# Kernel optimization log

Measured on AMD Instinct MI355X. Metric: run time of the kernel, lower is better.

The kernel has to match this reference:

```python
import jax, jax.numpy as jnp
import numpy as np

TOPK_CONF = 100   # cfg.nms_top_k_conf
TOPK_IOU = 15     # cfg.nms_top_k_iou
IOU_GAUSS = (32, 32)  # cfg.iou_gauss_dim
EPS = 1e-6        # cfg.positive


def unnormal_gaussian(mask_shape, loc):
    """loc: [..., 4] = (cx, cy, w, h) in [0,1). Returns [..., H, W] unnormalized gaussians."""
    H, W = mask_shape
    ys = (jnp.arange(H, dtype=loc.dtype) + 0.5) / H  # [H]
    xs = (jnp.arange(W, dtype=loc.dtype) + 0.5) / W  # [W]
    cx, cy = loc[..., 0], loc[..., 1]
    sx = jnp.abs(loc[..., 2]) * 0.5 + 1e-3
    sy = jnp.abs(loc[..., 3]) * 0.5 + 1e-3
    dx2 = (xs - cx[..., None]) ** 2 / (2.0 * sx[..., None] ** 2)  # [..., W]
    dy2 = (ys - cy[..., None]) ** 2 / (2.0 * sy[..., None] ** 2)  # [..., H]
    return jnp.exp(-(dy2[..., :, None] + dx2[..., None, :]))      # [..., H, W]


def setup_inputs() -> dict:
    key = jax.random.key(0)
    k1, k2, k3, k4, k5 = jax.random.split(key, 5)
    B, P, C, M = 4, 19248, 81, 32
    original = jax.random.normal(k1, (B, 3, 550, 550), dtype=jnp.float32)
    loc = jax.random.uniform(k2, (B, P, 4), dtype=jnp.float32)  # cx,cy,w,h in [0,1)
    conf = jax.random.normal(k3, (B, P, C), dtype=jnp.float32)
    mask = jax.random.normal(k4, (B, P, M), dtype=jnp.float32)
    proto = jax.random.normal(k5, (B, 138, 138, M), dtype=jnp.float32)
    return {"original": original, "loc": loc, "conf": conf, "mask": mask, "proto": proto}


def reference(original, loc, conf, mask, proto):
    B, H, W = original.shape[0], original.shape[2], original.shape[3]
    # class-1 foreground confidence after softmax over classes
    conf1 = jax.nn.softmax(conf, axis=2)[:, :, 1]  # [B, P]

    # ---- detect(): top-k by conf, pairwise gaussian IoU, keep lowest-overlap boxes ----
    order = jnp.argsort(-conf1, axis=-1)[:, :TOPK_CONF]                    # [B, K]
    sconf = jnp.take_along_axis(conf1, order, axis=1)                      # [B, K]
    sloc = jnp.take_along_axis(loc, order[..., None], axis=1)              # [B, K, 4]
    smask = jnp.take_along_axis(mask, order[..., None], axis=1)            # [B, K, Mdim]

    gauss = unnormal_gaussian(IOU_GAUSS, sloc)                             # [B, K, G, G]
    g_rows = gauss[:, None, :, :, :]                                       # broadcast [B,1,K,G,G]
    g_cols = gauss[:, :, None, :, :]                                       # broadcast [B,K,1,G,G]
    inter = jnp.sum(jnp.minimum(g_rows, g_cols), axis=(-2, -1))            # [B, K, K]
    union = jnp.sum(jnp.maximum(g_rows, g_cols), axis=(-2, -1))            # [B, K, K]
    gauss_iou = inter / union
    iou_max = jnp.max(jnp.triu(gauss_iou, k=1), axis=1)                    # [B, K]
    keep = jnp.argsort(iou_max, axis=-1)[:, :TOPK_IOU]                     # [B, Kk]

    kloc = jnp.take_along_axis(sloc, keep[..., None], axis=1)              # [B, Kk, 4]
    kmask = jnp.take_along_axis(smask, keep[..., None], axis=1)            # [B, Kk, Mdim]
    kconf = jnp.take_along_axis(sconf, keep, axis=1)                       # [B, Kk]

    # ---- VarianceLoss ----
    Hp, Wp = proto.shape[1], proto.shape[2]
    ug = unnormal_gaussian((Hp, Wp), kloc)                                 # [B, Kk, Hp, Wp]
    assembled = jax.nn.sigmoid(jnp.einsum('bhwm,bkm->bkhw', proto, kmask)) # lincomb + sigmoid
    attention = assembled * ug
    mask_conf = attention * kconf[:, :, None, None]                        # einsum('abcd,ab->abcd')
    denom = jnp.sum(mask_conf, axis=1, keepdims=True) + EPS
    final_conf = 1.0 - jnp.sum(mask_conf ** 2 / denom, axis=1)             # [B, Hp, Wp]
    final_conf = jnp.where(jnp.isnan(final_conf), 0.0, final_conf)

    resized = jax.image.resize(final_conf, (B, H, W), method='bilinear')   # [B, H, W]
    total_conf = jnp.sum(resized, axis=0)                                  # [H, W]
    weighted_mean = jnp.einsum('bchw,bhw->chw', original, resized)         # [C, H, W]
    squared_diff = (original - weighted_mean) ** 2
    weighted_diff = squared_diff * resized[:, None, :, :]                  # einsum('abcd,acd->abcd')
    weighted_var = weighted_diff / (total_conf + EPS)
    return jnp.sum(weighted_var) / 100.0
```

## Files before the change

### kernel.cpp

```cpp
#include <hip/hip_runtime.h>
#include <math.h>

#define B 4
#define P 19248
#define C 81
#define M 32
#define K1 100
#define K2 15
#define G 32
#define HP 138
#define HO 550
#define FEPS 1e-6f

#define NBUCKET 8192
#define CAP 2048

#define RROW 128
#define RSP 83

#define TI 16
#define NT 7
#define NTP 28
#define CH 128
#define NCH 8
#define SP 132

__global__ __launch_bounds__(128) void k_conf1(const float* __restrict__ conf,
                                               float* __restrict__ conf1) {
    int row0 = blockIdx.x * RROW;
    int nrows = min(RROW, B * P - row0);
    int tid = threadIdx.x;
    __shared__ float s_rows[RROW * RSP];
    const float* src = conf + (size_t)row0 * C;
    int total = nrows * C;
    for (int i = tid; i < total; i += 128) {
        int r = i / C, c2 = i - r * C;
        s_rows[r * RSP + c2] = src[i];
    }
    __syncthreads();
    if (tid < nrows) {
        const float* rw = &s_rows[tid * RSP];
        float m = rw[0];
#pragma unroll
        for (int i = 1; i < C; ++i) m = fmaxf(m, rw[i]);
        float s = 0.f, e1 = 0.f;
#pragma unroll
        for (int i = 0; i < C; ++i) {
            float e = expf(rw[i] - m);
            s += e;
            if (i == 1) e1 = e;
        }
        conf1[row0 + tid] = e1 / s;
    }
}

__global__ __launch_bounds__(1024) void k_hist(const float* __restrict__ conf1,
                                               unsigned int* __restrict__ ghist) {
    int b = blockIdx.y;
    int tid = threadIdx.x;
    __shared__ unsigned int lh[NBUCKET];
    for (int i = tid; i < NBUCKET; i += 1024) lh[i] = 0;
    __syncthreads();
    int p0 = blockIdx.x * (P / 8);
    for (int p = p0 + tid; p < p0 + P / 8; p += 1024) {
        unsigned int bits = __float_as_uint(conf1[(size_t)b * P + p]);
        atomicAdd(&lh[bits >> 17], 1u);
    }
    __syncthreads();
    for (int i = tid; i < NBUCKET; i += 1024) {
        unsigned int v = lh[i];
        if (v) atomicAdd(&ghist[b * NBUCKET + i], v);
    }
}

__global__ __launch_bounds__(1024) void k_select(
    const unsigned int* __restrict__ ghist, const float* __restrict__ conf1,
    const float* __restrict__ loc, const float* __restrict__ mask,
    float* __restrict__ sconf, float* __restrict__ sloc, float* __restrict__ smask) {
    int b = blockIdx.x;
    int tid = threadIdx.x;
    __shared__ unsigned int hist[NBUCKET];
    __shared__ unsigned int gsum_[1024];
    __shared__ unsigned int g2[64];
    __shared__ unsigned long long s_keys[CAP];
    __shared__ int s_T;
    __shared__ int s_cnt;
    __shared__ int   s_order[K1];
    __shared__ float s_conf[K1];

    for (int i = tid; i < NBUCKET; i += 1024) hist[i] = ghist[b * NBUCKET + i];
    if (tid == 0) s_cnt = 0;
    __syncthreads();
    {
        unsigned int gs = 0;
#pragma unroll
        for (int i = 0; i < 8; ++i) gs += hist[tid * 8 + i];
        gsum_[tid] = gs;
    }
    __syncthreads();
    if (tid < 64) {
        unsigned int gs = 0;
#pragma unroll
        for (int i = 0; i < 16; ++i) gs += gsum_[tid * 16 + i];
        g2[tid] = gs;
    }
    __syncthreads();
    if (tid < 64) {
        unsigned int v1 = g2[tid];
        unsigned int s1 = v1;
#pragma unroll
        for (int o = 1; o < 64; o <<= 1) {
            unsigned int x = __shfl_down(s1, o, 64);
            if (tid + o < 64) s1 += x;
        }
        unsigned long long m1 = __ballot((int)s1 >= K1);
        int S = 63 - __builtin_clzll(m1);
        int cum1 = (int)__shfl(s1, S, 64) - (int)__shfl(v1, S, 64);

        unsigned int v2 = (tid < 16) ? gsum_[S * 16 + tid] : 0u;
        unsigned int s2 = v2;
#pragma unroll
        for (int o = 1; o < 16; o <<= 1) {
            unsigned int x = __shfl_down(s2, o, 64);
            if (tid + o < 16) s2 += x;
        }
        unsigned long long m2 = __ballot((tid < 16) && (cum1 + (int)s2 >= K1));
        int r2 = 63 - __builtin_clzll(m2);
        int gI = S * 16 + r2;
        int cum2 = cum1 + (int)__shfl(s2, r2, 64) - (int)__shfl(v2, r2, 64);

        unsigned int v3 = (tid < 8) ? hist[gI * 8 + tid] : 0u;
        unsigned int s3 = v3;
#pragma unroll
        for (int o = 1; o < 8; o <<= 1) {
            unsigned int x = __shfl_down(s3, o, 64);
            if (tid + o < 8) s3 += x;
        }
        unsigned long long m3 = __ballot((tid < 8) && (cum2 + (int)s3 >= K1));
        int r3 = 63 - __builtin_clzll(m3);
        if (tid == 0) s_T = gI * 8 + r3;
    }
    __syncthreads();

    int T = s_T;
    for (int p = tid; p < P; p += 1024) {
        unsigned int bits = __float_as_uint(conf1[(size_t)b * P + p]);
        if ((int)(bits >> 17) >= T) {
            int pos = atomicAdd(&s_cnt, 1);
            if (pos < CAP)
                s_keys[pos] = ((unsigned long long)bits << 32)
                            | (unsigned int)(0xFFFFFFFFu - (unsigned int)p);
        }
    }
    __syncthreads();
    int nc = min(s_cnt, CAP);
    int ncp = (nc + 7) & ~7;
    if (tid < ncp - nc) s_keys[nc + tid] = 0ULL;
    __syncthreads();

    for (int t = tid; t < nc; t += 1024) {
        unsigned long long mk = s_keys[t];
        int rank = 0;
#pragma unroll 8
        for (int i = 0; i < ncp; ++i) rank += (s_keys[i] > mk);
        if (rank < K1) {
            s_order[rank] = (int)(0xFFFFFFFFu - (unsigned int)(mk & 0xFFFFFFFFu));
            s_conf[rank] = __uint_as_float((unsigned int)(mk >> 32));
        }
    }
    __syncthreads();

    for (int t = tid; t < K1; t += 1024) sconf[b * K1 + t] = s_conf[t];
    for (int t = tid; t < K1 * 4; t += 1024) {
        int k = t >> 2, d = t & 3;
        sloc[(b * K1 + k) * 4 + d] = loc[((size_t)b * P + s_order[k]) * 4 + d];
    }
    for (int t = tid; t < K1 * M; t += 1024) {
        int k = t >> 5, d = t & 31;
        smask[(b * K1 + k) * M + d] = mask[((size_t)b * P + s_order[k]) * M + d];
    }
}

__global__ void k_gauss(const float* __restrict__ sloc, float* __restrict__ gauss) {
    int bk = blockIdx.x;
    const float* l = sloc + bk * 4;
    float cx = l[0], cy = l[1];
    float sx = fabsf(l[2]) * 0.5f + 0.001f;
    float sy = fabsf(l[3]) * 0.5f + 0.001f;
    float dsx = 2.f * sx * sx;
    float dsy = 2.f * sy * sy;
    for (int p = threadIdx.x; p < G * G; p += 256) {
        int y = p >> 5, x = p & 31;
        float xs = (x + 0.5f) / (float)G;
        float ys = (y + 0.5f) / (float)G;
        float dx2 = (xs - cx) * (xs - cx) / dsx;
        float dy2 = (ys - cy) * (ys - cy) / dsy;
        gauss[(size_t)bk * (G * G) + p] = expf(-(dy2 + dx2));
    }
}

__global__ __launch_bounds__(256) void k_iou_tile(
    const float* __restrict__ gauss, float* __restrict__ Ibuf,
    float* __restrict__ Ubuf) {
    int ch = blockIdx.x;
    int tp = blockIdx.y;
    int b  = blockIdx.z;
    int ti = 0, rem = tp;
    while (rem >= NT - ti) { rem -= NT - ti; ++ti; }
    int tj = ti + rem;

    __shared__ __align__(16) float As[TI][SP];
    __shared__ __align__(16) float Bs[TI][SP];

    int tid = threadIdx.x;
    for (int idx = tid; idx < TI * (CH / 4); idx += 256) {
        int g = idx >> 5, v = idx & 31;
        int gi = ti * TI + g;
        float4 f = make_float4(0.f, 0.f, 0.f, 0.f);
        if (gi < K1)
            f = *(const float4*)(gauss + ((size_t)(b * K1 + gi) << 10) + ch * CH + v * 4);
        *(float4*)(&As[g][v * 4]) = f;
        int gj = tj * TI + g;
        float4 h = make_float4(0.f, 0.f, 0.f, 0.f);
        if (gj < K1)
            h = *(const float4*)(gauss + ((size_t)(b * K1 + gj) << 10) + ch * CH + v * 4);
        *(float4*)(&Bs[g][v * 4]) = h;
    }
    __syncthreads();

    int li = tid >> 4, lj = tid & 15;
    int i = ti * TI + li, j = tj * TI + lj;
    if (i < j && j < K1) {
        const float4* ar = (const float4*)(&As[li][0]);
        const float4* br = (const float4*)(&Bs[lj][0]);
        float inter = 0.f, uni = 0.f;
#pragma unroll
        for (int p = 0; p < CH / 4; ++p) {
            float4 a = ar[p], c = br[p];
            inter += fminf(a.x, c.x) + fminf(a.y, c.y)
                   + fminf(a.z, c.z) + fminf(a.w, c.w);
            uni   += fmaxf(a.x, c.x) + fmaxf(a.y, c.y)
                   + fmaxf(a.z, c.z) + fmaxf(a.w, c.w);
        }
        atomicAdd(&Ibuf[(b * K1 + i) * K1 + j], inter);
        atomicAdd(&Ubuf[(b * K1 + i) * K1 + j], uni);
    }
}

__global__ void k_combine(const float* __restrict__ Ibuf, const float* __restrict__ Ubuf,
                          unsigned int* __restrict__ ioumax) {
    int gid = blockIdx.x * 256 + threadIdx.x;
    if (gid >= B * K1 * K1) return;
    int b = gid / (K1 * K1);
    int rem = gid - b * K1 * K1;
    int i = rem / K1, j = rem % K1;
    if (i >= j) return;
    float iou = Ibuf[gid] / Ubuf[gid];
    atomicMax(&ioumax[b * K1 + j], __float_as_uint(iou));
}

__global__ void k_keep(const unsigned int* __restrict__ ioumax,
                       const float* __restrict__ sloc, const float* __restrict__ smask,
                       const float* __restrict__ sconf,
                       float* __restrict__ kloc, float* __restrict__ kmask,
                       float* __restrict__ kconf) {
    int b = blockIdx.x;
    int lane = threadIdx.x;
    float v0 = (lane < K1)      ? __uint_as_float(ioumax[b * K1 + lane])      : INFINITY;
    float v1 = (lane + 64 < K1) ? __uint_as_float(ioumax[b * K1 + lane + 64]) : INFINITY;
    __shared__ int s_keep[K2];
    for (int k = 0; k < K2; ++k) {
        float bv; int bi;
        if (v0 <= v1) { bv = v0; bi = lane; }
        else          { bv = v1; bi = lane + 64; }
#pragma unroll
        for (int o = 32; o; o >>= 1) {
            float ov = __shfl_xor(bv, o, 64);
            int   oi = __shfl_xor(bi, o, 64);
            if (ov < bv || (ov == bv && oi < bi)) { bv = ov; bi = oi; }
        }
        if (bi == lane)           v0 = INFINITY;
        else if (bi == lane + 64) v1 = INFINITY;
        if (lane == 0) s_keep[k] = bi;
    }
    __syncthreads();
    for (int t = lane; t < K2 * M; t += 64) {
        int k = t >> 5, d = t & 31;
        kmask[(b * K2 + k) * M + d] = smask[(b * K1 + s_keep[k]) * M + d];
    }
    for (int t = lane; t < K2 * 4; t += 64) {
        int k = t >> 2, d = t & 3;
        kloc[(b * K2 + k) * 4 + d] = sloc[(b * K1 + s_keep[k]) * 4 + d];
    }
    if (lane < K2) kconf[b * K2 + lane] = sconf[b * K1 + s_keep[lane]];
}

__global__ __launch_bounds__(256) void k_fconf(
    const float* __restrict__ proto, const float* __restrict__ kloc,
    const float* __restrict__ kmask, const float* __restrict__ kconf,
    float* __restrict__ fconf) {
    int b = blockIdx.y;
    int px0 = blockIdx.x * 256;
    int tid = threadIdx.x;
    __shared__ float s_pv[256][M + 1];
    __shared__ float s_km[K2][M];
    __shared__ float s_loc[K2][4];
    __shared__ float s_cf[K2];
    for (int t = tid; t < K2 * M; t += 256) s_km[t >> 5][t & 31] = kmask[b * K2 * M + t];
    for (int t = tid; t < K2 * 4; t += 256) s_loc[t >> 2][t & 3] = kloc[b * K2 * 4 + t];
    if (tid < K2) s_cf[tid] = kconf[b * K2 + tid];

    int nvalid = min(256, HP * HP - px0);
    const float4* pr4 = (const float4*)(proto + ((size_t)b * (HP * HP) + px0) * M);
    for (int idx = tid; idx < nvalid * (M / 4); idx += 256) {
        float4 f = pr4[idx];
        int q = idx >> 3, v = idx & 7;
        s_pv[q][v * 4 + 0] = f.x;
        s_pv[q][v * 4 + 1] = f.y;
        s_pv[q][v * 4 + 2] = f.z;
        s_pv[q][v * 4 + 3] = f.w;
    }
    __syncthreads();

    if (tid < nvalid) {
        int p = px0 + tid;
        int h = p / HP, w = p % HP;
        float pv[M];
#pragma unroll
        for (int m = 0; m < M; ++m) pv[m] = s_pv[tid][m];
        float ys = (h + 0.5f) / (float)HP;
        float xs = (w + 0.5f) / (float)HP;
        float sum_a = 0.f, sum_a2 = 0.f;
#pragma unroll 1
        for (int k = 0; k < K2; ++k) {
            float d = 0.f;
#pragma unroll
            for (int m = 0; m < M; ++m) d += pv[m] * s_km[k][m];
            float sig = 1.f / (1.f + expf(-d));
            float cx = s_loc[k][0], cy = s_loc[k][1];
            float sx = fabsf(s_loc[k][2]) * 0.5f + 0.001f;
            float sy = fabsf(s_loc[k][3]) * 0.5f + 0.001f;
            float dx2 = (xs - cx) * (xs - cx) / (2.f * sx * sx);
            float dy2 = (ys - cy) * (ys - cy) / (2.f * sy * sy);
            float ug = expf(-(dy2 + dx2));
            float a = sig * ug * s_cf[k];
            sum_a  += a;
            sum_a2 += a * a;
        }
        float fin = 1.f - sum_a2 / (sum_a + FEPS);
        if (!(fin == fin)) fin = 0.f;
        fconf[(size_t)b * HP * HP + p] = fin;
    }
}

__global__ void k_reduce(const float* __restrict__ fconf, const float* __restrict__ original,
                         float* __restrict__ acc, unsigned int* __restrict__ count,
                         float* __restrict__ out) {
    int idx = blockIdx.x * 256 + threadIdx.x;
    float contrib = 0.f;
    if (idx < HO * HO) {
        int y = idx / HO, x = idx % HO;
        const float scale = (float)HP / (float)HO;
        float fy = (y + 0.5f) * scale - 0.5f;
        float fx = (x + 0.5f) * scale - 0.5f;
        float y0f = floorf(fy), x0f = floorf(fx);
        float wy = fy - y0f, wx = fx - x0f;
        int y0 = (int)y0f, x0 = (int)x0f;
        int iy0 = max(y0, 0), iy1 = min(y0 + 1, HP - 1);
        int ix0 = max(x0, 0), ix1 = min(x0 + 1, HP - 1);
        float r[B];
#pragma unroll
        for (int b = 0; b < B; ++b) {
            const float* F = fconf + (size_t)b * HP * HP;
            float v00 = F[iy0 * HP + ix0], v01 = F[iy0 * HP + ix1];
            float v10 = F[iy1 * HP + ix0], v11 = F[iy1 * HP + ix1];
            r[b] = (1.f - wy) * ((1.f - wx) * v00 + wx * v01)
                 +        wy  * ((1.f - wx) * v10 + wx * v11);
        }
        float t = r[0] + r[1] + r[2] + r[3];
        float s = 0.f;
#pragma unroll
        for (int c = 0; c < 3; ++c) {
            float o[B], wm = 0.f;
#pragma unroll
            for (int b = 0; b < B; ++b) {
                o[b] = original[(((size_t)b * 3 + c) * HO + y) * HO + x];
                wm += o[b] * r[b];
            }
#pragma unroll
            for (int b = 0; b < B; ++b) {
                float d = o[b] - wm;
                s += d * d * r[b];
            }
        }
        contrib = s / (t + FEPS);
    }
    __shared__ float red[256];
    red[threadIdx.x] = contrib;
    __syncthreads();
    for (int off = 128; off; off >>= 1) {
        if (threadIdx.x < off) red[threadIdx.x] += red[threadIdx.x + off];
        __syncthreads();
    }
    if (threadIdx.x == 0) {
        atomicAdd(acc, red[0]);
        __threadfence();
        unsigned int prev = atomicAdd(count, 1u);
        if (prev == gridDim.x - 1) {
            __threadfence();
            float total = atomicAdd(acc, 0.0f);
            out[0] = total / 100.f;
        }
    }
}

extern "C" void kernel_launch(void* const* d_in, const int* in_sizes, int n_in,
                              void* d_out, int out_size, void* d_ws, size_t ws_size,
                              hipStream_t stream) {
    (void)in_sizes; (void)n_in; (void)out_size; (void)ws_size;
    const float* original = (const float*)d_in[0];
    const float* loc      = (const float*)d_in[1];
    const float* conf     = (const float*)d_in[2];
    const float* mask     = (const float*)d_in[3];
    const float* proto    = (const float*)d_in[4];

    char* ws = (char*)d_ws;
    size_t off = 0;
    auto alloc = [&](size_t bytes) -> void* {
        void* p = ws + off;
        off += (bytes + 255) & ~(size_t)255;
        return p;
    };
    unsigned int* ghist = (unsigned int*)alloc((size_t)B * NBUCKET * sizeof(unsigned int));
    float* Ibuf         = (float*)alloc((size_t)B * K1 * K1 * sizeof(float));
    float* Ubuf         = (float*)alloc((size_t)B * K1 * K1 * sizeof(float));
    unsigned int* iomax = (unsigned int*)alloc((size_t)B * K1 * sizeof(unsigned int));
    float*        acc   = (float*)alloc(sizeof(float));
    unsigned int* count = (unsigned int*)alloc(sizeof(unsigned int));
    size_t zero_bytes = off;
    float* conf1        = (float*)alloc((size_t)B * P * sizeof(float));
    float* sconf        = (float*)alloc((size_t)B * K1 * sizeof(float));
    float* sloc         = (float*)alloc((size_t)B * K1 * 4 * sizeof(float));
    float* smask        = (float*)alloc((size_t)B * K1 * M * sizeof(float));
    float* gauss        = (float*)alloc((size_t)B * K1 * G * G * sizeof(float));
    float* kloc         = (float*)alloc((size_t)B * K2 * 4 * sizeof(float));
    float* kmask        = (float*)alloc((size_t)B * K2 * M * sizeof(float));
    float* kconf        = (float*)alloc((size_t)B * K2 * sizeof(float));
    float* fconf        = (float*)alloc((size_t)B * HP * HP * sizeof(float));

    hipMemsetAsync(ws, 0, zero_bytes, stream);

    k_conf1<<<(B * P + RROW - 1) / RROW, 128, 0, stream>>>(conf, conf1);
    dim3 gh(8, B);
    k_hist<<<gh, 1024, 0, stream>>>(conf1, ghist);
    k_select<<<B, 1024, 0, stream>>>(ghist, conf1, loc, mask, sconf, sloc, smask);
    k_gauss<<<B * K1, 256, 0, stream>>>(sloc, gauss);
    dim3 g4(NCH, NTP, B);
    k_iou_tile<<<g4, 256, 0, stream>>>(gauss, Ibuf, Ubuf);
    k_combine<<<(B * K1 * K1 + 255) / 256, 256, 0, stream>>>(Ibuf, Ubuf, iomax);
    k_keep<<<B, 64, 0, stream>>>(iomax, sloc, smask, sconf, kloc, kmask, kconf);
    dim3 g6((HP * HP + 255) / 256, B);
    k_fconf<<<g6, 256, 0, stream>>>(proto, kloc, kmask, kconf, fconf);
    k_reduce<<<(HO * HO + 255) / 256, 256, 0, stream>>>(fconf, original, acc, count,
                                                        (float*)d_out);
}
```

Measured before the change: 186.8 us.

## Fuse selection pipeline kernels and drop memset and intermediate gaussian buffer

Collapses the launch chain by removing the memset, the separate histogram kernel, the gaussian kernel and the combine kernel. Zeroing moves into k_select, which now builds the per-batch histogram itself in one block. Gaussians are recomputed inside the IoU tile loader, and the IoU max and keep selection are merged into one k_nms kernel using shared-memory atomics. Softmax is rewritten as one wave per row with shuffle reductions. This reduces launch count and global traffic, at the cost of a serial histogram over P elements with only 4 blocks and redundant exp work in the IoU tiles.

```diff
diff --git a/kernel.cpp b/kernel.cpp
--- a/kernel.cpp
+++ b/kernel.cpp
@@ -15,9 +15,6 @@
 #define NBUCKET 8192
 #define CAP 2048
 
-#define RROW 128
-#define RSP 83
-
 #define TI 16
 #define NT 7
 #define NTP 28
@@ -25,58 +22,31 @@
 #define NCH 8
 #define SP 132
 
-__global__ __launch_bounds__(128) void k_conf1(const float* __restrict__ conf,
-                                               float* __restrict__ conf1) {
-    int row0 = blockIdx.x * RROW;
-    int nrows = min(RROW, B * P - row0);
-    int tid = threadIdx.x;
-    __shared__ float s_rows[RROW * RSP];
-    const float* src = conf + (size_t)row0 * C;
-    int total = nrows * C;
-    for (int i = tid; i < total; i += 128) {
-        int r = i / C, c2 = i - r * C;
-        s_rows[r * RSP + c2] = src[i];
-    }
-    __syncthreads();
-    if (tid < nrows) {
-        const float* rw = &s_rows[tid * RSP];
-        float m = rw[0];
-#pragma unroll
-        for (int i = 1; i < C; ++i) m = fmaxf(m, rw[i]);
-        float s = 0.f, e1 = 0.f;
-#pragma unroll
-        for (int i = 0; i < C; ++i) {
-            float e = expf(rw[i] - m);
-            s += e;
-            if (i == 1) e1 = e;
-        }
-        conf1[row0 + tid] = e1 / s;
-    }
-}
-
-__global__ __launch_bounds__(1024) void k_hist(const float* __restrict__ conf1,
-                                               unsigned int* __restrict__ ghist) {
-    int b = blockIdx.y;
-    int tid = threadIdx.x;
-    __shared__ unsigned int lh[NBUCKET];
-    for (int i = tid; i < NBUCKET; i += 1024) lh[i] = 0;
-    __syncthreads();
-    int p0 = blockIdx.x * (P / 8);
-    for (int p = p0 + tid; p < p0 + P / 8; p += 1024) {
-        unsigned int bits = __float_as_uint(conf1[(size_t)b * P + p]);
-        atomicAdd(&lh[bits >> 17], 1u);
-    }
-    __syncthreads();
-    for (int i = tid; i < NBUCKET; i += 1024) {
-        unsigned int v = lh[i];
-        if (v) atomicAdd(&ghist[b * NBUCKET + i], v);
-    }
+__global__ void k_conf1(const float* __restrict__ conf, float* __restrict__ conf1) {
+    int gid  = blockIdx.x * blockDim.x + threadIdx.x;
+    int wave = gid >> 6;
+    int lane = threadIdx.x & 63;
+    if (wave >= B * P) return;
+    const float* row = conf + (size_t)wave * C;
+    float x0 = (lane < C)      ? row[lane]      : -INFINITY;
+    float x1 = (lane + 64 < C) ? row[lane + 64] : -INFINITY;
+    float m = fmaxf(x0, x1);
+#pragma unroll
+    for (int o = 32; o; o >>= 1) m = fmaxf(m, __shfl_xor(m, o, 64));
+    float s = 0.f;
+    if (lane < C)      s += expf(x0 - m);
+    if (lane + 64 < C) s += expf(x1 - m);
+#pragma unroll
+    for (int o = 32; o; o >>= 1) s += __shfl_xor(s, o, 64);
+    if (lane == 0) conf1[wave] = expf(row[1] - m) / s;
 }
 
 __global__ __launch_bounds__(1024) void k_select(
-    const unsigned int* __restrict__ ghist, const float* __restrict__ conf1,
-    const float* __restrict__ loc, const float* __restrict__ mask,
-    float* __restrict__ sconf, float* __restrict__ sloc, float* __restrict__ smask) {
+    const float* __restrict__ conf1, const float* __restrict__ loc,
+    const float* __restrict__ mask,
+    float* __restrict__ sconf, float* __restrict__ sloc, float* __restrict__ smask,
+    float* __restrict__ Ibuf, float* __restrict__ Ubuf,
+    float* __restrict__ acc, unsigned int* __restrict__ count) {
     int b = blockIdx.x;
     int tid = threadIdx.x;
     __shared__ unsigned int hist[NBUCKET];
@@ -88,8 +58,20 @@
     __shared__ int   s_order[K1];
     __shared__ float s_conf[K1];
 
-    for (int i = tid; i < NBUCKET; i += 1024) hist[i] = ghist[b * NBUCKET + i];
+    for (int i = tid; i < K1 * K1; i += 1024) {
+        Ibuf[b * K1 * K1 + i] = 0.f;
+        Ubuf[b * K1 * K1 + i] = 0.f;
+    }
+    if (b == 0 && tid == 0) { *acc = 0.f; *count = 0u; }
+
+    for (int i = tid; i < NBUCKET; i += 1024) hist[i] = 0;
     if (tid == 0) s_cnt = 0;
+    __syncthreads();
+
+    for (int p = tid; p < P; p += 1024) {
+        unsigned int bits = __float_as_uint(conf1[(size_t)b * P + p]);
+        atomicAdd(&hist[bits >> 17], 1u);
+    }
     __syncthreads();
     {
         unsigned int gs = 0;
@@ -181,26 +163,8 @@
     }
 }
 
-__global__ void k_gauss(const float* __restrict__ sloc, float* __restrict__ gauss) {
-    int bk = blockIdx.x;
-    const float* l = sloc + bk * 4;
-    float cx = l[0], cy = l[1];
-    float sx = fabsf(l[2]) * 0.5f + 0.001f;
-    float sy = fabsf(l[3]) * 0.5f + 0.001f;
-    float dsx = 2.f * sx * sx;
-    float dsy = 2.f * sy * sy;
-    for (int p = threadIdx.x; p < G * G; p += 256) {
-        int y = p >> 5, x = p & 31;
-        float xs = (x + 0.5f) / (float)G;
-        float ys = (y + 0.5f) / (float)G;
-        float dx2 = (xs - cx) * (xs - cx) / dsx;
-        float dy2 = (ys - cy) * (ys - cy) / dsy;
-        gauss[(size_t)bk * (G * G) + p] = expf(-(dy2 + dx2));
-    }
-}
-
-__global__ __launch_bounds__(256) void k_iou_tile(
-    const float* __restrict__ gauss, float* __restrict__ Ibuf,
+__global__ __launch_bounds__(256) void k_iou(
+    const float* __restrict__ sloc, float* __restrict__ Ibuf,
     float* __restrict__ Ubuf) {
     int ch = blockIdx.x;
     int tp = blockIdx.y;
@@ -215,16 +179,34 @@
     int tid = threadIdx.x;
     for (int idx = tid; idx < TI * (CH / 4); idx += 256) {
         int g = idx >> 5, v = idx & 31;
-        int gi = ti * TI + g;
-        float4 f = make_float4(0.f, 0.f, 0.f, 0.f);
-        if (gi < K1)
-            f = *(const float4*)(gauss + ((size_t)(b * K1 + gi) << 10) + ch * CH + v * 4);
-        *(float4*)(&As[g][v * 4]) = f;
-        int gj = tj * TI + g;
-        float4 h = make_float4(0.f, 0.f, 0.f, 0.f);
-        if (gj < K1)
-            h = *(const float4*)(gauss + ((size_t)(b * K1 + gj) << 10) + ch * CH + v * 4);
-        *(float4*)(&Bs[g][v * 4]) = h;
+        int px0 = ch * CH + v * 4;
+#pragma unroll
+        for (int pass = 0; pass < 2; ++pass) {
+            int gg = (pass ? tj : ti) * TI + g;
+            float4 f = make_float4(0.f, 0.f, 0.f, 0.f);
+            if (gg < K1) {
+                const float* l = sloc + (b * K1 + gg) * 4;
+                float cx = l[0], cy = l[1];
+                float sx = fabsf(l[2]) * 0.5f + 0.001f;
+                float sy = fabsf(l[3]) * 0.5f + 0.001f;
+                float dsx = 2.f * sx * sx;
+                float dsy = 2.f * sy * sy;
+                float vals[4];
+#pragma unroll
+                for (int c = 0; c < 4; ++c) {
+                    int px = px0 + c;
+                    int y = px >> 5, x = px & 31;
+                    float xs = (x + 0.5f) / (float)G;
+                    float ys = (y + 0.5f) / (float)G;
+                    float dx2 = (xs - cx) * (xs - cx) / dsx;
+                    float dy2 = (ys - cy) * (ys - cy) / dsy;
+                    vals[c] = expf(-(dy2 + dx2));
+                }
+                f = make_float4(vals[0], vals[1], vals[2], vals[3]);
+            }
+            if (pass) *(float4*)(&Bs[g][v * 4]) = f;
+            else      *(float4*)(&As[g][v * 4]) = f;
+        }
     }
     __syncthreads();
 
@@ -247,52 +229,55 @@
     }
 }
 
-__global__ void k_combine(const float* __restrict__ Ibuf, const float* __restrict__ Ubuf,
-                          unsigned int* __restrict__ ioumax) {
-    int gid = blockIdx.x * 256 + threadIdx.x;
-    if (gid >= B * K1 * K1) return;
-    int b = gid / (K1 * K1);
-    int rem = gid - b * K1 * K1;
-    int i = rem / K1, j = rem % K1;
-    if (i >= j) return;
-    float iou = Ibuf[gid] / Ubuf[gid];
-    atomicMax(&ioumax[b * K1 + j], __float_as_uint(iou));
-}
-
-__global__ void k_keep(const unsigned int* __restrict__ ioumax,
-                       const float* __restrict__ sloc, const float* __restrict__ smask,
-                       const float* __restrict__ sconf,
-                       float* __restrict__ kloc, float* __restrict__ kmask,
-                       float* __restrict__ kconf) {
+__global__ __launch_bounds__(256) void k_nms(
+    const float* __restrict__ Ibuf, const float* __restrict__ Ubuf,
+    const float* __restrict__ sloc, const float* __restrict__ smask,
+    const float* __restrict__ sconf,
+    float* __restrict__ kloc, float* __restrict__ kmask,
+    float* __restrict__ kconf) {
     int b = blockIdx.x;
-    int lane = threadIdx.x;
-    float v0 = (lane < K1)      ? __uint_as_float(ioumax[b * K1 + lane])      : INFINITY;
-    float v1 = (lane + 64 < K1) ? __uint_as_float(ioumax[b * K1 + lane + 64]) : INFINITY;
+    int tid = threadIdx.x;
+    __shared__ unsigned int s_iomax[K1];
     __shared__ int s_keep[K2];
-    for (int k = 0; k < K2; ++k) {
-        float bv; int bi;
-        if (v0 <= v1) { bv = v0; bi = lane; }
-        else          { bv = v1; bi = lane + 64; }
-#pragma unroll
-        for (int o = 32; o; o >>= 1) {
-            float ov = __shfl_xor(bv, o, 64);
-            int   oi = __shfl_xor(bi, o, 64);
-            if (ov < bv || (ov == bv && oi < bi)) { bv = ov; bi = oi; }
-        }
-        if (bi == lane)           v0 = INFINITY;
-        else if (bi == lane + 64) v1 = INFINITY;
-        if (lane == 0) s_keep[k] = bi;
-    }
-    __syncthreads();
-    for (int t = lane; t < K2 * M; t += 64) {
+    for (int i = tid; i < K1; i += 256) s_iomax[i] = 0u;
+    __syncthreads();
+    for (int pr = tid; pr < K1 * K1; pr += 256) {
+        int i = pr / K1, j = pr - (pr / K1) * K1;
+        if (i < j) {
+            float iou = Ibuf[b * K1 * K1 + pr] / Ubuf[b * K1 * K1 + pr];
+            atomicMax(&s_iomax[j], __float_as_uint(iou));
+        }
+    }
+    __syncthreads();
+    if (tid < 64) {
+        int lane = tid;
+        float v0 = (lane < K1)      ? __uint_as_float(s_iomax[lane])      : INFINITY;
+        float v1 = (lane + 64 < K1) ? __uint_as_float(s_iomax[lane + 64]) : INFINITY;
+        for (int k = 0; k < K2; ++k) {
+            float bv; int bi;
+            if (v0 <= v1) { bv = v0; bi = lane; }
+            else          { bv = v1; bi = lane + 64; }
+#pragma unroll
+            for (int o = 32; o; o >>= 1) {
+                float ov = __shfl_xor(bv, o, 64);
+                int   oi = __shfl_xor(bi, o, 64);
+                if (ov < bv || (ov == bv && oi < bi)) { bv = ov; bi = oi; }
+            }
+            if (bi == lane)           v0 = INFINITY;
+            else if (bi == lane + 64) v1 = INFINITY;
+            if (lane == 0) s_keep[k] = bi;
+        }
+    }
+    __syncthreads();
+    for (int t = tid; t < K2 * M; t += 256) {
         int k = t >> 5, d = t & 31;
         kmask[(b * K2 + k) * M + d] = smask[(b * K1 + s_keep[k]) * M + d];
     }
-    for (int t = lane; t < K2 * 4; t += 64) {
+    for (int t = tid; t < K2 * 4; t += 256) {
         int k = t >> 2, d = t & 3;
         kloc[(b * K2 + k) * 4 + d] = sloc[(b * K1 + s_keep[k]) * 4 + d];
     }
-    if (lane < K2) kconf[b * K2 + lane] = sconf[b * K1 + s_keep[lane]];
+    if (tid < K2) kconf[b * K2 + tid] = sconf[b * K1 + s_keep[tid]];
 }
 
 __global__ __launch_bounds__(256) void k_fconf(
@@ -431,34 +416,25 @@
         off += (bytes + 255) & ~(size_t)255;
         return p;
     };
-    unsigned int* ghist = (unsigned int*)alloc((size_t)B * NBUCKET * sizeof(unsigned int));
-    float* Ibuf         = (float*)alloc((size_t)B * K1 * K1 * sizeof(float));
-    float* Ubuf         = (float*)alloc((size_t)B * K1 * K1 * sizeof(float));
-    unsigned int* iomax = (unsigned int*)alloc((size_t)B * K1 * sizeof(unsigned int));
-    float*        acc   = (float*)alloc(sizeof(float));
-    unsigned int* count = (unsigned int*)alloc(sizeof(unsigned int));
-    size_t zero_bytes = off;
     float* conf1        = (float*)alloc((size_t)B * P * sizeof(float));
     float* sconf        = (float*)alloc((size_t)B * K1 * sizeof(float));
     float* sloc         = (float*)alloc((size_t)B * K1 * 4 * sizeof(float));
     float* smask        = (float*)alloc((size_t)B * K1 * M * sizeof(float));
-    float* gauss        = (float*)alloc((size_t)B * K1 * G * G * sizeof(float));
+    float* Ibuf         = (float*)alloc((size_t)B * K1 * K1 * sizeof(float));
+    float* Ubuf         = (float*)alloc((size_t)B * K1 * K1 * sizeof(float));
     float* kloc         = (float*)alloc((size_t)B * K2 * 4 * sizeof(float));
     float* kmask        = (float*)alloc((size_t)B * K2 * M * sizeof(float));
     float* kconf        = (float*)alloc((size_t)B * K2 * sizeof(float));
     float* fconf        = (float*)alloc((size_t)B * HP * HP * sizeof(float));
-
-    hipMemsetAsync(ws, 0, zero_bytes, stream);
-
-    k_conf1<<<(B * P + RROW - 1) / RROW, 128, 0, stream>>>(conf, conf1);
-    dim3 gh(8, B);
-    k_hist<<<gh, 1024, 0, stream>>>(conf1, ghist);
-    k_select<<<B, 1024, 0, stream>>>(ghist, conf1, loc, mask, sconf, sloc, smask);
-    k_gauss<<<B * K1, 256, 0, stream>>>(sloc, gauss);
+    float* acc          = (float*)alloc(sizeof(float));
+    unsigned int* count = (unsigned int*)alloc(sizeof(unsigned int));
+
+    k_conf1<<<(B * P) / 4, 256, 0, stream>>>(conf, conf1);
+    k_select<<<B, 1024, 0, stream>>>(conf1, loc, mask, sconf, sloc, smask,
+                                     Ibuf, Ubuf, acc, count);
     dim3 g4(NCH, NTP, B);
-    k_iou_tile<<<g4, 256, 0, stream>>>(gauss, Ibuf, Ubuf);
-    k_combine<<<(B * K1 * K1 + 255) / 256, 256, 0, stream>>>(Ibuf, Ubuf, iomax);
-    k_keep<<<B, 64, 0, stream>>>(iomax, sloc, smask, sconf, kloc, kmask, kconf);
+    k_iou<<<g4, 256, 0, stream>>>(sloc, Ibuf, Ubuf);
+    k_nms<<<B, 256, 0, stream>>>(Ibuf, Ubuf, sloc, smask, sconf, kloc, kmask, kconf);
     dim3 g6((HP * HP + 255) / 256, B);
     k_fconf<<<g6, 256, 0, stream>>>(proto, kloc, kmask, kconf, fconf);
     k_reduce<<<(HO * HO + 255) / 256, 256, 0, stream>>>(fconf, original, acc, count,
```

Measured after the change: 196.1 us. +5.0%, slower.
